# Kernel tuning notes

Hardware: AMD Instinct MI355X
Metric: run time of the kernel (lower is better)

## Reference

```python
import jax, jax.numpy as jnp
import numpy as np

N_NODES = 50000   # gnn_nodes_num
N_EDGES = 800000  # avg degree 16
HIDDEN = 64       # hidden_channels
BATCH_Y = 2048    # |y|


def setup_inputs() -> dict:
    key = jax.random.key(0)
    ks = jax.random.split(key, 16)
    s = 0.05
    H = HIDDEN
    return {
        "x": jnp.arange(N_NODES, dtype=jnp.int32),
        "edge_index": jax.random.randint(ks[0], (2, N_EDGES), 0, N_NODES, dtype=jnp.int32),
        "y": jax.random.randint(ks[1], (BATCH_Y,), 0, N_NODES, dtype=jnp.int32),
        # learned params
        "emb": jax.random.normal(ks[2], (N_NODES, H), dtype=jnp.float32) * s,
        "Wq": jax.random.normal(ks[3], (H, H), dtype=jnp.float32) * s,
        "bq": jnp.zeros((H,), dtype=jnp.float32),
        "Wk": jax.random.normal(ks[4], (H, H), dtype=jnp.float32) * s,
        "bk": jnp.zeros((H,), dtype=jnp.float32),
        "Wv": jax.random.normal(ks[5], (H, H), dtype=jnp.float32) * s,
        "bv": jnp.zeros((H,), dtype=jnp.float32),
        "Ws": jax.random.normal(ks[6], (H, H), dtype=jnp.float32) * s,  # root/skip lin
        "bs": jnp.zeros((H,), dtype=jnp.float32),
        "W1": jax.random.normal(ks[7], (H, N_NODES), dtype=jnp.float32) * s,
        "b1": jnp.zeros((N_NODES,), dtype=jnp.float32),
    }


def reference(x, edge_index, y, emb, Wq, bq, Wk, bk, Wv, bv, Ws, bs, W1, b1):
    H = Wq.shape[1]
    h = emb[x]                                  # [N, H] embedding lookup
    src, dst = edge_index[0], edge_index[1]

    # TransformerConv (heads=1, root_weight=True): per-node projections
    q = h @ Wq + bq                             # [N, H]
    k = h @ Wk + bk
    v = h @ Wv + bv

    # attention logits per edge, softmax grouped by destination node
    logits = jnp.sum(q[dst] * k[src], axis=-1) / jnp.sqrt(jnp.float32(H))  # [E]
    m = jax.ops.segment_max(logits, dst, num_segments=N_NODES)             # [N]
    e = jnp.exp(logits - m[dst])
    denom = jax.ops.segment_sum(e, dst, num_segments=N_NODES)              # [N]
    alpha = e / denom[dst]                                                 # [E]

    agg = jax.ops.segment_sum(alpha[:, None] * v[src], dst, num_segments=N_NODES)
    out = agg + h @ Ws + bs                     # [N, H] GAT output

    # for each node u: sum of out[dst] over edges with src == u  (vectorized
    # form of the original per-y boolean-mask loop), then gather at y
    neigh = jax.ops.segment_sum(out[dst], src, num_segments=N_NODES)       # [N, H]
    new_x = neigh[y]                            # [B, H]

    return jax.nn.softmax(new_x @ W1 + b1, axis=-1)  # [B, N]
```

## Files before the change

### kernel.cpp

```cpp
#include <hip/hip_runtime.h>
#include <math.h>

#define NN 50000
#define NE 800000
#define HH 64
#define NB 2048
#define NTILES 784
#define NPAD 50176
#define NSTRIPE 64
#define NBLK 256

typedef __attribute__((ext_vector_type(8))) short bf16x8;
typedef __attribute__((ext_vector_type(4))) float f32x4;

__device__ inline ushort f2bf(float f) {
  uint u = __float_as_uint(f);
  uint r = (u + 0x7fffu + ((u >> 16) & 1u)) >> 16;
  return (ushort)r;
}
__device__ inline float bf2f(uint u) { return __uint_as_float(u << 16); }

__global__ __launch_bounds__(256) void k_prep(
    const float* __restrict__ W1,
    const float* __restrict__ Wq, const float* __restrict__ Wk,
    const float* __restrict__ Wv, const float* __restrict__ Ws,
    ushort* __restrict__ W1T, ushort* __restrict__ WT,
    int* cnt_d, int* cnt_s, char* flag, char* ymark, int* bar)
{
  int i = blockIdx.x * 256 + threadIdx.x;
  if (i < NN) { cnt_d[i] = 0; cnt_s[i] = 0; flag[i] = 0; ymark[i] = 0; }
  if (i == 0) *bar = 0;
  if (i < 4 * HH * HH) {
    int m = i >> 12, rem = i & 4095;
    int c = rem >> 6, kk = rem & 63;
    const float* W = (m == 0) ? Wq : (m == 1) ? Wk : (m == 2) ? Wv : Ws;
    WT[i] = f2bf(W[kk * HH + c]);
  }
  if (i < NPAD) {
    uint4 o[8];
    ushort* op = (ushort*)o;
    if (i < NN) {
#pragma unroll
      for (int k = 0; k < HH; ++k) op[k] = f2bf(W1[(size_t)k * NN + i]);
    } else {
#pragma unroll
      for (int k = 0; k < HH; ++k) op[k] = 0;
    }
    uint4* dst = (uint4*)(W1T + (size_t)i * HH);
#pragma unroll
    for (int j = 0; j < 8; ++j) dst[j] = o[j];
  }
}

__global__ __launch_bounds__(256) void k_mark(const int* __restrict__ y,
                                              char* __restrict__ ymark) {
  int i = blockIdx.x * 256 + threadIdx.x;
  if (i < NB) ymark[y[i]] = 1;
}

__global__ __launch_bounds__(256) void k_hist(const int* __restrict__ src,
                                              const int* __restrict__ dst,
                                              const char* __restrict__ ymark,
                                              int* cnt_s, int* cnt_d,
                                              char* __restrict__ flag,
                                              int* __restrict__ rank_d,
                                              int* __restrict__ rank_s) {
  int e = blockIdx.x * 256 + threadIdx.x;
  if (e < NE) {
    int s = src[e], d = dst[e];
    rank_d[e] = atomicAdd(&cnt_d[d], 1);
    if (ymark[s]) {
      rank_s[e] = atomicAdd(&cnt_s[s], 1);
      flag[d] = 1;
    } else {
      rank_s[e] = -1;
    }
  }
}

__global__ __launch_bounds__(1024) void k_scan(
    const int* __restrict__ cnt_d, int* indptr_d,
    const int* __restrict__ cnt_s, int* indptr_s)
{
  const int* cnt = (blockIdx.x == 0) ? cnt_d : cnt_s;
  int* indptr    = (blockIdx.x == 0) ? indptr_d : indptr_s;
  __shared__ int sums[1024];
  const int CH = (NN + 1023) / 1024;
  int t = threadIdx.x;
  int begin = t * CH;
  int end = begin + CH; if (end > NN) end = NN;
  int s = 0;
  for (int i = begin; i < end; ++i) s += cnt[i];
  sums[t] = s;
  __syncthreads();
  for (int off = 1; off < 1024; off <<= 1) {
    int val = (t >= off) ? sums[t - off] : 0;
    __syncthreads();
    sums[t] += val;
    __syncthreads();
  }
  int prefix = (t == 0) ? 0 : sums[t - 1];
  for (int i = begin; i < end; ++i) {
    indptr[i] = prefix;
    prefix += cnt[i];
  }
  if (t == 0) indptr[NN] = sums[1023];
}

__global__ __launch_bounds__(256) void k_qkvs(
    const int* __restrict__ x, const float* __restrict__ emb,
    const ushort* __restrict__ WT,
    const float* __restrict__ bq, const float* __restrict__ bk,
    const float* __restrict__ bv, const float* __restrict__ bs,
    ushort* __restrict__ qb, ushort* __restrict__ kb, ushort* __restrict__ vb,
    float* __restrict__ hs)
{
  int l = threadIdx.x & 63, w = threadIdx.x >> 6;
  int lr = l & 15, lk = l >> 4;
  int r0 = blockIdx.x * 64;
  const ushort* wt = WT + w * HH * HH;
  const float* B = (w == 0) ? bq : (w == 1) ? bk : (w == 2) ? bv : bs;

  bf16x8 b[2][4];
#pragma unroll
  for (int kt = 0; kt < 2; ++kt)
#pragma unroll
    for (int nt = 0; nt < 4; ++nt)
      b[kt][nt] = *(const bf16x8*)(wt + (nt * 16 + lr) * HH + kt * 32 + lk * 8);

  bf16x8 a[2][4];
#pragma unroll
  for (int mt = 0; mt < 4; ++mt) {
    int row = r0 + mt * 16 + lr;
    int g = (row < NN) ? x[row] : 0;
    const float* hp = emb + (size_t)g * HH;
#pragma unroll
    for (int kt = 0; kt < 2; ++kt) {
      float4 f0 = *(const float4*)(hp + kt * 32 + lk * 8);
      float4 f1 = *(const float4*)(hp + kt * 32 + lk * 8 + 4);
      bf16x8 af;
      af[0] = f2bf(f0.x); af[1] = f2bf(f0.y); af[2] = f2bf(f0.z); af[3] = f2bf(f0.w);
      af[4] = f2bf(f1.x); af[5] = f2bf(f1.y); af[6] = f2bf(f1.z); af[7] = f2bf(f1.w);
      a[kt][mt] = af;
    }
  }

  f32x4 acc[4][4];
  const f32x4 z4 = {0.f, 0.f, 0.f, 0.f};
#pragma unroll
  for (int mt = 0; mt < 4; ++mt)
#pragma unroll
    for (int nt = 0; nt < 4; ++nt) acc[mt][nt] = z4;
#pragma unroll
  for (int kt = 0; kt < 2; ++kt)
#pragma unroll
    for (int mt = 0; mt < 4; ++mt)
#pragma unroll
      for (int nt = 0; nt < 4; ++nt)
        acc[mt][nt] = __builtin_amdgcn_mfma_f32_16x16x32_bf16(a[kt][mt], b[kt][nt], acc[mt][nt], 0, 0, 0);

  if (w < 3) {
    ushort* Db = (w == 0) ? qb : (w == 1) ? kb : vb;
#pragma unroll
    for (int mt = 0; mt < 4; ++mt)
#pragma unroll
      for (int r = 0; r < 4; ++r) {
        int row = r0 + mt * 16 + lk * 4 + r;
        if (row < NN) {
#pragma unroll
          for (int nt = 0; nt < 4; ++nt) {
            int c = nt * 16 + lr;
            Db[(size_t)row * HH + c] = f2bf(acc[mt][nt][r] + B[c]);
          }
        }
      }
  } else {
#pragma unroll
    for (int mt = 0; mt < 4; ++mt)
#pragma unroll
      for (int r = 0; r < 4; ++r) {
        int row = r0 + mt * 16 + lk * 4 + r;
        if (row < NN) {
#pragma unroll
          for (int nt = 0; nt < 4; ++nt) {
            int c = nt * 16 + lr;
            hs[(size_t)row * HH + c] = acc[mt][nt][r] + B[c];
          }
        }
      }
  }
}

__global__ __launch_bounds__(256) void k_efill(
    const int* __restrict__ src, const int* __restrict__ dst,
    const ushort* __restrict__ qb, const ushort* __restrict__ kb,
    const char* __restrict__ flag,
    const int* __restrict__ indptr_s, const int* __restrict__ indptr_d,
    const int* __restrict__ rank_d, const int* __restrict__ rank_s,
    int* __restrict__ dstlist_s, int2* __restrict__ slot_d)
{
  int gid = blockIdx.x * 256 + threadIdx.x;
  int e = gid >> 3;
  int lane = gid & 7;
  if (e >= NE) return;
  int s = src[e], d = dst[e];
  bool fd = flag[d];
  float p = 0.f;
  if (fd) {
    uint4 qa = *(const uint4*)(qb + (size_t)d * HH + lane * 8);
    uint4 ka = *(const uint4*)(kb + (size_t)s * HH + lane * 8);
    p += bf2f(qa.x & 0xffffu) * bf2f(ka.x & 0xffffu) + bf2f(qa.x >> 16) * bf2f(ka.x >> 16);
    p += bf2f(qa.y & 0xffffu) * bf2f(ka.y & 0xffffu) + bf2f(qa.y >> 16) * bf2f(ka.y >> 16);
    p += bf2f(qa.z & 0xffffu) * bf2f(ka.z & 0xffffu) + bf2f(qa.z >> 16) * bf2f(ka.z >> 16);
    p += bf2f(qa.w & 0xffffu) * bf2f(ka.w & 0xffffu) + bf2f(qa.w >> 16) * bf2f(ka.w >> 16);
    p += __shfl_xor(p, 4);
    p += __shfl_xor(p, 2);
    p += __shfl_xor(p, 1);
  }
  if (lane == 0) {
    if (fd) {
      int pd = indptr_d[d] + rank_d[e];
      int2 sl; sl.x = s; sl.y = __float_as_int(p * 0.125f);
      slot_d[pd] = sl;
    }
    int rs = rank_s[e];
    if (rs >= 0) dstlist_s[indptr_s[s] + rs] = d;
  }
}

__global__ __launch_bounds__(256) void k_agg(
    const int* __restrict__ indptr_d, const int2* __restrict__ slot_d,
    const ushort* __restrict__ vb, const char* __restrict__ flag,
    float* __restrict__ hs)
{
  int w = (blockIdx.x * 256 + threadIdx.x) >> 6;
  int lane = threadIdx.x & 63;
  if (w >= NN) return;
  if (!flag[w]) return;
  int beg = indptr_d[w], end = indptr_d[w + 1];
  if (beg == end) return;
  float den = 0.f, acc = 0.f;
  for (int j = beg; j < end; ++j) {
    int2 sl = slot_d[j];
    float p = __expf(__int_as_float(sl.y));
    den += p;
    acc = fmaf(p, bf2f((uint)vb[(size_t)sl.x * HH + lane]), acc);
  }
  hs[(size_t)w * HH + lane] += acc / den;
}

__global__ __launch_bounds__(256) void k_newx(
    const int* __restrict__ y, const int* __restrict__ indptr_s,
    const int* __restrict__ dstlist_s, const float* __restrict__ outn,
    ushort* __restrict__ nxbf)
{
  int w = (blockIdx.x * 256 + threadIdx.x) >> 6;
  int lane = threadIdx.x & 63;
  if (w >= NB) return;
  int u = y[w];
  int beg = indptr_s[u], end = indptr_s[u + 1];
  float acc = 0.f;
  for (int j = beg; j < end; ++j) acc += outn[(size_t)dstlist_s[j] * HH + lane];
  nxbf[w * HH + lane] = f2bf(acc);
}

#define LOADA(A, t) do { int bn0_ = (t) * 64;                                    \
  _Pragma("unroll") for (int kt = 0; kt < 2; ++kt)                               \
  _Pragma("unroll") for (int nt = 0; nt < 4; ++nt)                               \
    A[kt][nt] = *(const bf16x8*)(w1t + (size_t)(bn0_ + nt * 16 + lr) * HH + kt * 32 + lk * 8); \
} while (0)

#define MFMA16(A, acc) do {                                                      \
  _Pragma("unroll") for (int kt = 0; kt < 2; ++kt)                               \
  _Pragma("unroll") for (int mt = 0; mt < 4; ++mt)                               \
  _Pragma("unroll") for (int nt = 0; nt < 4; ++nt)                               \
    acc[mt][nt] = __builtin_amdgcn_mfma_f32_16x16x32_bf16(A[kt][nt], bm[kt][mt], acc[mt][nt], 0, 0, 0); \
} while (0)

#define PROCA(A, t) do { int bn0_ = (t) * 64;                                    \
  f32x4 acc[4][4];                                                               \
  _Pragma("unroll") for (int mt = 0; mt < 4; ++mt)                               \
  _Pragma("unroll") for (int nt = 0; nt < 4; ++nt) acc[mt][nt] = z4;             \
  MFMA16(A, acc);                                                                \
  _Pragma("unroll") for (int nt = 0; nt < 4; ++nt) {                             \
    int n0 = bn0_ + nt * 16 + lk * 4;                                            \
    if (n0 < NN) {                                                               \
      f32x4 bb = *(const f32x4*)(b1 + n0);                                       \
      _Pragma("unroll") for (int mt = 0; mt < 4; ++mt)                           \
      _Pragma("unroll") for (int r = 0; r < 4; ++r)                              \
        se[mt] += __expf(acc[mt][nt][r] + bb[r]);                                \
    } }                                                                          \
} while (0)

#define PROCB(A, t) do { int bn0_ = (t) * 64;                                    \
  f32x4 acc[4][4];                                                               \
  _Pragma("unroll") for (int mt = 0; mt < 4; ++mt)                               \
  _Pragma("unroll") for (int nt = 0; nt < 4; ++nt) acc[mt][nt] = z4;             \
  MFMA16(A, acc);                                                                \
  _Pragma("unroll") for (int nt = 0; nt < 4; ++nt) {                             \
    int n0 = bn0_ + nt * 16 + lk * 4;                                            \
    if (n0 < NN) {                                                               \
      f32x4 bb = *(const f32x4*)(b1 + n0);                                       \
      _Pragma("unroll") for (int mt = 0; mt < 4; ++mt) {                         \
        int row = bm0 + mt * 16 + lr;                                            \
        f32x4 vx;                                                                \
        _Pragma("unroll") for (int r = 0; r < 4; ++r)                            \
          vx[r] = __expf(acc[mt][nt][r] + bb[r]) * sv[mt];                       \
        __builtin_nontemporal_store(vx, (f32x4*)(out + (size_t)row * NN + n0));  \
      }                                                                          \
    } }                                                                          \
} while (0)

__global__ __launch_bounds__(512, 1) void k_final(
    const ushort* __restrict__ nxbf, const ushort* __restrict__ w1t,
    const float* __restrict__ b1, float* __restrict__ Spart,
    int* __restrict__ bar, float* __restrict__ out)
{
  __shared__ float sInvS[512];
  int tid = threadIdx.x;
  int l = tid & 63, w = tid >> 6;
  int lr = l & 15, lk = l >> 4;
  int rg = blockIdx.x >> 6;
  int st = blockIdx.x & 63;
  int bm0 = rg * 512 + w * 64;
  const f32x4 z4 = {0.f, 0.f, 0.f, 0.f};

  bf16x8 bm[2][4];
#pragma unroll
  for (int kt = 0; kt < 2; ++kt)
#pragma unroll
    for (int mt = 0; mt < 4; ++mt)
      bm[kt][mt] = *(const bf16x8*)(nxbf + (size_t)(bm0 + mt * 16 + lr) * HH + kt * 32 + lk * 8);

  float se[4];
#pragma unroll
  for (int mt = 0; mt < 4; ++mt) se[mt] = 0.f;

  {
    bf16x8 aA[2][4], aB[2][4];
    int t = st;
    LOADA(aA, t);
    while (true) {
      int t1 = t + NSTRIPE;
      if (t1 < NTILES) LOADA(aB, t1);
      PROCA(aA, t);
      if (t1 >= NTILES) break;
      int t2 = t1 + NSTRIPE;
      if (t2 < NTILES) LOADA(aA, t2);
      PROCA(aB, t1);
      if (t2 >= NTILES) break;
      t = t2;
    }
  }

#pragma unroll
  for (int mt = 0; mt < 4; ++mt) {
    float s = se[mt];
    s += __shfl_xor(s, 16);
    s += __shfl_xor(s, 32);
    if (lk == 0) {
      int row = bm0 + mt * 16 + lr;
      __hip_atomic_store(&Spart[row * NSTRIPE + st], s,
                         __ATOMIC_RELAXED, __HIP_MEMORY_SCOPE_AGENT);
    }
  }

  __threadfence();
  __syncthreads();
  if (tid == 0) {
    __hip_atomic_fetch_add(bar, 1, __ATOMIC_ACQ_REL, __HIP_MEMORY_SCOPE_AGENT);
    while (__hip_atomic_load(bar, __ATOMIC_ACQUIRE, __HIP_MEMORY_SCOPE_AGENT) < NBLK)
      __builtin_amdgcn_s_sleep(2);
  }
  __syncthreads();

  {
    int row = rg * 512 + tid;
    float s = 0.f;
    for (int j = 0; j < NSTRIPE; ++j)
      s += __hip_atomic_load(&Spart[row * NSTRIPE + j],
                             __ATOMIC_RELAXED, __HIP_MEMORY_SCOPE_AGENT);
    sInvS[tid] = 1.0f / s;
  }
  __syncthreads();

  float sv[4];
#pragma unroll
  for (int mt = 0; mt < 4; ++mt) sv[mt] = sInvS[w * 64 + mt * 16 + lr];

  {
    bf16x8 aA[2][4], aB[2][4];
    int t = st;
    LOADA(aA, t);
    while (true) {
      int t1 = t + NSTRIPE;
      if (t1 < NTILES) LOADA(aB, t1);
      PROCB(aA, t);
      if (t1 >= NTILES) break;
      int t2 = t1 + NSTRIPE;
      if (t2 < NTILES) LOADA(aA, t2);
      PROCB(aB, t1);
      if (t2 >= NTILES) break;
      t = t2;
    }
  }
}

extern "C" void kernel_launch(void* const* d_in, const int* in_sizes, int n_in,
                              void* d_out, int out_size, void* d_ws, size_t ws_size,
                              hipStream_t stream)
{
  const int* x   = (const int*)d_in[0];
  const int* src = (const int*)d_in[1];
  const int* dst = src + NE;
  const int* y   = (const int*)d_in[2];
  const float* emb = (const float*)d_in[3];
  const float* Wq = (const float*)d_in[4];  const float* bq = (const float*)d_in[5];
  const float* Wk = (const float*)d_in[6];  const float* bk = (const float*)d_in[7];
  const float* Wv = (const float*)d_in[8];  const float* bv = (const float*)d_in[9];
  const float* Ws = (const float*)d_in[10]; const float* bs = (const float*)d_in[11];
  const float* W1 = (const float*)d_in[12]; const float* b1 = (const float*)d_in[13];
  float* out = (float*)d_out;

  char* wsb = (char*)d_ws;
  ushort* nxbf  = (ushort*)wsb;
  ushort* w1t   = (ushort*)(wsb + 262144);
  float*  Spart = (float*)(wsb + 6684672);
  int*    bar   = (int*)(wsb + 7208960);
  const size_t PERS  = 7209088;
  const size_t BIGSZ = 46400000;
  char* big = (ws_size >= PERS + BIGSZ) ? (wsb + PERS) : (char*)d_out;
  ushort* qb     = (ushort*)(big + 0);
  ushort* kb     = (ushort*)(big + 6400000);
  ushort* vb     = (ushort*)(big + 12800000);
  float*  hs     = (float*)(big + 19200000);
  int2*   slot_d = (int2*)(big + 32000000);
  int* dstlist_s = (int*)(big + 38400000);
  int* rank_d    = (int*)(big + 38700000);
  int* rank_s    = (int*)(big + 41900000);
  int* cnt_d     = (int*)(big + 45100000);
  int* cnt_s     = (int*)(big + 45300000);
  int* indptr_d  = (int*)(big + 45500000);
  int* indptr_s  = (int*)(big + 45700064);
  char* flag     = (char*)(big + 45900128);
  char* ymark    = (char*)(big + 45950176);
  ushort* WT     = (ushort*)(big + 46000224);

  k_prep<<<dim3(224), dim3(256), 0, stream>>>(W1, Wq, Wk, Wv, Ws, w1t, WT,
                                              cnt_d, cnt_s, flag, ymark, bar);
  k_mark<<<dim3(8), dim3(256), 0, stream>>>(y, ymark);
  k_hist<<<dim3(3125), dim3(256), 0, stream>>>(src, dst, ymark, cnt_s, cnt_d,
                                               flag, rank_d, rank_s);
  k_scan<<<dim3(2), dim3(1024), 0, stream>>>(cnt_d, indptr_d, cnt_s, indptr_s);
  k_qkvs<<<dim3(782), dim3(256), 0, stream>>>(x, emb, WT, bq, bk, bv, bs,
                                              qb, kb, vb, hs);
  k_efill<<<dim3(25000), dim3(256), 0, stream>>>(src, dst, qb, kb, flag,
                                                 indptr_s, indptr_d, rank_d, rank_s,
                                                 dstlist_s, slot_d);
  k_agg<<<dim3(12500), dim3(256), 0, stream>>>(indptr_d, slot_d, vb, flag, hs);
  k_newx<<<dim3(512), dim3(256), 0, stream>>>(y, indptr_s, dstlist_s, hs, nxbf);
  k_final<<<dim3(NBLK), dim3(512), 0, stream>>>(nxbf, w1t, b1, Spart, bar, out);
}
```

Baseline: 512.9 us.

## Split fused softmax-GEMM into three kernels and stage output through LDS

Replaces the single persistent k_final kernel, which used a grid-wide spin barrier, with three launches. k_finA computes partial exp-sums, k_sinv reduces them to inverse row sums, and k_finB recomputes the GEMM and writes the normalized output. Each warp now owns 16 rows instead of 64, and the column range is split into 16 contiguous stripes of 49 tiles. k_finB transposes results through swizzled LDS so each lane stores contiguous row segments, in place of scattered nontemporal column stores. This removes the barrier and improves store coalescing, at the cost of two extra launches, more reloads of W1T per row, and plain rather than nontemporal stores.

Result: no change. 505.8 us (-1.4%).

```diff
diff --git a/kernel.cpp b/kernel.cpp
--- a/kernel.cpp
+++ b/kernel.cpp
@@ -5,10 +5,10 @@
 #define NE 800000
 #define HH 64
 #define NB 2048
-#define NTILES 784
 #define NPAD 50176
-#define NSTRIPE 64
-#define NBLK 256
+#define NST 16
+#define TPS 49
+#define NSUP 12
 
 typedef __attribute__((ext_vector_type(8))) short bf16x8;
 typedef __attribute__((ext_vector_type(4))) float f32x4;
@@ -25,11 +25,10 @@
     const float* __restrict__ Wq, const float* __restrict__ Wk,
     const float* __restrict__ Wv, const float* __restrict__ Ws,
     ushort* __restrict__ W1T, ushort* __restrict__ WT,
-    int* cnt_d, int* cnt_s, char* flag, char* ymark, int* bar)
+    int* cnt_d, int* cnt_s, char* flag, char* ymark)
 {
   int i = blockIdx.x * 256 + threadIdx.x;
   if (i < NN) { cnt_d[i] = 0; cnt_s[i] = 0; flag[i] = 0; ymark[i] = 0; }
-  if (i == 0) *bar = 0;
   if (i < 4 * HH * HH) {
     int m = i >> 12, rem = i & 4095;
     int c = rem >> 6, kk = rem & 63;
@@ -270,138 +269,148 @@
     A[kt][nt] = *(const bf16x8*)(w1t + (size_t)(bn0_ + nt * 16 + lr) * HH + kt * 32 + lk * 8); \
 } while (0)
 
-#define MFMA16(A, acc) do {                                                      \
+#define MFMA8(A, acc) do {                                                       \
   _Pragma("unroll") for (int kt = 0; kt < 2; ++kt)                               \
-  _Pragma("unroll") for (int mt = 0; mt < 4; ++mt)                               \
   _Pragma("unroll") for (int nt = 0; nt < 4; ++nt)                               \
-    acc[mt][nt] = __builtin_amdgcn_mfma_f32_16x16x32_bf16(A[kt][nt], bm[kt][mt], acc[mt][nt], 0, 0, 0); \
+    acc[nt] = __builtin_amdgcn_mfma_f32_16x16x32_bf16(A[kt][nt], bm[kt], acc[nt], 0, 0, 0); \
 } while (0)
 
 #define PROCA(A, t) do { int bn0_ = (t) * 64;                                    \
-  f32x4 acc[4][4];                                                               \
-  _Pragma("unroll") for (int mt = 0; mt < 4; ++mt)                               \
-  _Pragma("unroll") for (int nt = 0; nt < 4; ++nt) acc[mt][nt] = z4;             \
-  MFMA16(A, acc);                                                                \
+  f32x4 acc[4];                                                                  \
+  _Pragma("unroll") for (int nt = 0; nt < 4; ++nt) acc[nt] = z4;                 \
+  MFMA8(A, acc);                                                                 \
   _Pragma("unroll") for (int nt = 0; nt < 4; ++nt) {                             \
     int n0 = bn0_ + nt * 16 + lk * 4;                                            \
     if (n0 < NN) {                                                               \
       f32x4 bb = *(const f32x4*)(b1 + n0);                                       \
-      _Pragma("unroll") for (int mt = 0; mt < 4; ++mt)                           \
       _Pragma("unroll") for (int r = 0; r < 4; ++r)                              \
-        se[mt] += __expf(acc[mt][nt][r] + bb[r]);                                \
+        se += __expf(acc[nt][r] + bb[r]);                                        \
     } }                                                                          \
 } while (0)
 
-#define PROCB(A, t) do { int bn0_ = (t) * 64;                                    \
-  f32x4 acc[4][4];                                                               \
-  _Pragma("unroll") for (int mt = 0; mt < 4; ++mt)                               \
-  _Pragma("unroll") for (int nt = 0; nt < 4; ++nt) acc[mt][nt] = z4;             \
-  MFMA16(A, acc);                                                                \
-  _Pragma("unroll") for (int nt = 0; nt < 4; ++nt) {                             \
-    int n0 = bn0_ + nt * 16 + lk * 4;                                            \
-    if (n0 < NN) {                                                               \
-      f32x4 bb = *(const f32x4*)(b1 + n0);                                       \
-      _Pragma("unroll") for (int mt = 0; mt < 4; ++mt) {                         \
-        int row = bm0 + mt * 16 + lr;                                            \
-        f32x4 vx;                                                                \
-        _Pragma("unroll") for (int r = 0; r < 4; ++r)                            \
-          vx[r] = __expf(acc[mt][nt][r] + bb[r]) * sv[mt];                       \
-        __builtin_nontemporal_store(vx, (f32x4*)(out + (size_t)row * NN + n0));  \
-      }                                                                          \
-    } }                                                                          \
-} while (0)
-
-__global__ __launch_bounds__(512, 1) void k_final(
+__global__ __launch_bounds__(256) void k_finA(
     const ushort* __restrict__ nxbf, const ushort* __restrict__ w1t,
-    const float* __restrict__ b1, float* __restrict__ Spart,
-    int* __restrict__ bar, float* __restrict__ out)
-{
-  __shared__ float sInvS[512];
+    const float* __restrict__ b1, float* __restrict__ Spart)
+{
   int tid = threadIdx.x;
   int l = tid & 63, w = tid >> 6;
   int lr = l & 15, lk = l >> 4;
-  int rg = blockIdx.x >> 6;
-  int st = blockIdx.x & 63;
-  int bm0 = rg * 512 + w * 64;
+  int b = blockIdx.x;
+  int st = ((b & 7) << 1) | ((b >> 3) & 1);
+  int r0 = (b >> 4) * 64 + w * 16;
+  int tile0 = st * TPS;
   const f32x4 z4 = {0.f, 0.f, 0.f, 0.f};
 
-  bf16x8 bm[2][4];
+  bf16x8 bm[2];
 #pragma unroll
   for (int kt = 0; kt < 2; ++kt)
-#pragma unroll
-    for (int mt = 0; mt < 4; ++mt)
-      bm[kt][mt] = *(const bf16x8*)(nxbf + (size_t)(bm0 + mt * 16 + lr) * HH + kt * 32 + lk * 8);
-
-  float se[4];
-#pragma unroll
-  for (int mt = 0; mt < 4; ++mt) se[mt] = 0.f;
-
+    bm[kt] = *(const bf16x8*)(nxbf + (size_t)(r0 + lr) * HH + kt * 32 + lk * 8);
+
+  float se = 0.f;
   {
-    bf16x8 aA[2][4], aB[2][4];
-    int t = st;
-    LOADA(aA, t);
-    while (true) {
-      int t1 = t + NSTRIPE;
-      if (t1 < NTILES) LOADA(aB, t1);
-      PROCA(aA, t);
-      if (t1 >= NTILES) break;
-      int t2 = t1 + NSTRIPE;
-      if (t2 < NTILES) LOADA(aA, t2);
-      PROCA(aB, t1);
-      if (t2 >= NTILES) break;
-      t = t2;
-    }
-  }
-
-#pragma unroll
-  for (int mt = 0; mt < 4; ++mt) {
-    float s = se[mt];
-    s += __shfl_xor(s, 16);
-    s += __shfl_xor(s, 32);
-    if (lk == 0) {
-      int row = bm0 + mt * 16 + lr;
-      __hip_atomic_store(&Spart[row * NSTRIPE + st], s,
-                         __ATOMIC_RELAXED, __HIP_MEMORY_SCOPE_AGENT);
-    }
-  }
-
-  __threadfence();
-  __syncthreads();
-  if (tid == 0) {
-    __hip_atomic_fetch_add(bar, 1, __ATOMIC_ACQ_REL, __HIP_MEMORY_SCOPE_AGENT);
-    while (__hip_atomic_load(bar, __ATOMIC_ACQUIRE, __HIP_MEMORY_SCOPE_AGENT) < NBLK)
-      __builtin_amdgcn_s_sleep(2);
-  }
-  __syncthreads();
-
+    bf16x8 A0[2][4], A1[2][4];
+    LOADA(A0, tile0);
+#pragma unroll 4
+    for (int t = 0; t < TPS - 1; t += 2) {
+      LOADA(A1, tile0 + t + 1);
+      PROCA(A0, tile0 + t);
+      LOADA(A0, tile0 + t + 2);
+      PROCA(A1, tile0 + t + 1);
+    }
+    PROCA(A0, tile0 + TPS - 1);
+  }
+  se += __shfl_xor(se, 16);
+  se += __shfl_xor(se, 32);
+  if (lk == 0) Spart[(r0 + lr) * NST + st] = se;
+}
+
+__global__ __launch_bounds__(256) void k_sinv(const float* __restrict__ Spart,
+                                              float* __restrict__ Sinv) {
+  int r = blockIdx.x * 256 + threadIdx.x;
+  if (r < NB) {
+    float s = 0.f;
+#pragma unroll
+    for (int j = 0; j < NST; ++j) s += Spart[r * NST + j];
+    Sinv[r] = 1.0f / s;
+  }
+}
+
+#define PROCB1(A, t, tt) do { int bn0_ = (t) * 64;                               \
+  f32x4 acc[4];                                                                  \
+  _Pragma("unroll") for (int nt = 0; nt < 4; ++nt) acc[nt] = z4;                 \
+  MFMA8(A, acc);                                                                 \
+  _Pragma("unroll") for (int nt = 0; nt < 4; ++nt) {                             \
+    int n0 = bn0_ + nt * 16 + lk * 4;                                            \
+    f32x4 bb = (n0 < NN) ? *(const f32x4*)(b1 + n0) : z4;                        \
+    f32x4 ev;                                                                    \
+    _Pragma("unroll") for (int r = 0; r < 4; ++r)                                \
+      ev[r] = __expf(acc[nt][r] + bb[r]) * sv;                                   \
+    int col = (tt) * 64 + nt * 16 + lk * 4;                                      \
+    *(f32x4*)&lw[lr * 256 + (col ^ ((lr & 7) << 2))] = ev;                       \
+  }                                                                              \
+} while (0)
+
+__global__ __launch_bounds__(256) void k_finB(
+    const ushort* __restrict__ nxbf, const ushort* __restrict__ w1t,
+    const float* __restrict__ b1, const float* __restrict__ Sinv,
+    float* __restrict__ out)
+{
+  __shared__ float lt[4 * 4096];
+  int tid = threadIdx.x;
+  int l = tid & 63, w = tid >> 6;
+  int lr = l & 15, lk = l >> 4;
+  int b = blockIdx.x;
+  int st = ((b & 7) << 1) | ((b >> 3) & 1);
+  int r0 = (b >> 4) * 64 + w * 16;
+  int tile0 = st * TPS;
+  const f32x4 z4 = {0.f, 0.f, 0.f, 0.f};
+  float* lw = &lt[w * 4096];
+
+  bf16x8 bm[2];
+#pragma unroll
+  for (int kt = 0; kt < 2; ++kt)
+    bm[kt] = *(const bf16x8*)(nxbf + (size_t)(r0 + lr) * HH + kt * 32 + lk * 8);
+
+  float sv = Sinv[r0 + lr];
+
+  for (int sb = 0; sb < NSUP; ++sb) {
+    int tb = tile0 + sb * 4;
+    bf16x8 A0[2][4], A1[2][4];
+    LOADA(A0, tb);
+    LOADA(A1, tb + 1);
+    PROCB1(A0, tb, 0);
+    LOADA(A0, tb + 2);
+    PROCB1(A1, tb + 1, 1);
+    LOADA(A1, tb + 3);
+    PROCB1(A0, tb + 2, 2);
+    PROCB1(A1, tb + 3, 3);
+    int nbase = tb * 64 + l * 4;
+#pragma unroll
+    for (int i = 0; i < 16; ++i) {
+      f32x4 vx = *(const f32x4*)&lw[i * 256 + ((l * 4) ^ ((i & 7) << 2))];
+      if (nbase < NN)
+        *(f32x4*)(out + (size_t)(r0 + i) * NN + nbase) = vx;
+    }
+  }
   {
-    int row = rg * 512 + tid;
-    float s = 0.f;
-    for (int j = 0; j < NSTRIPE; ++j)
-      s += __hip_atomic_load(&Spart[row * NSTRIPE + j],
-                             __ATOMIC_RELAXED, __HIP_MEMORY_SCOPE_AGENT);
-    sInvS[tid] = 1.0f / s;
-  }
-  __syncthreads();
-
-  float sv[4];
-#pragma unroll
-  for (int mt = 0; mt < 4; ++mt) sv[mt] = sInvS[w * 64 + mt * 16 + lr];
-
-  {
-    bf16x8 aA[2][4], aB[2][4];
-    int t = st;
-    LOADA(aA, t);
-    while (true) {
-      int t1 = t + NSTRIPE;
-      if (t1 < NTILES) LOADA(aB, t1);
-      PROCB(aA, t);
-      if (t1 >= NTILES) break;
-      int t2 = t1 + NSTRIPE;
-      if (t2 < NTILES) LOADA(aA, t2);
-      PROCB(aB, t1);
-      if (t2 >= NTILES) break;
-      t = t2;
+    int t = tile0 + TPS - 1;
+    int bn0 = t * 64;
+    bf16x8 A0[2][4];
+    LOADA(A0, t);
+    f32x4 acc[4];
+#pragma unroll
+    for (int nt = 0; nt < 4; ++nt) acc[nt] = z4;
+    MFMA8(A0, acc);
+#pragma unroll
+    for (int nt = 0; nt < 4; ++nt) {
+      int n0 = bn0 + nt * 16 + lk * 4;
+      if (n0 < NN) {
+        f32x4 bb = *(const f32x4*)(b1 + n0);
+        f32x4 vx;
+#pragma unroll
+        for (int r = 0; r < 4; ++r) vx[r] = __expf(acc[nt][r] + bb[r]) * sv;
+        *(f32x4*)(out + (size_t)(r0 + lr) * NN + n0) = vx;
+      }
     }
   }
 }
@@ -426,8 +435,8 @@
   ushort* nxbf  = (ushort*)wsb;
   ushort* w1t   = (ushort*)(wsb + 262144);
   float*  Spart = (float*)(wsb + 6684672);
-  int*    bar   = (int*)(wsb + 7208960);
-  const size_t PERS  = 7209088;
+  float*  Sinv  = (float*)(wsb + 6815744);
+  const size_t PERS  = 6823936;
   const size_t BIGSZ = 46400000;
   char* big = (ws_size >= PERS + BIGSZ) ? (wsb + PERS) : (char*)d_out;
   ushort* qb     = (ushort*)(big + 0);
@@ -447,7 +456,7 @@
   ushort* WT     = (ushort*)(big + 46000224);
 
   k_prep<<<dim3(224), dim3(256), 0, stream>>>(W1, Wq, Wk, Wv, Ws, w1t, WT,
-                                              cnt_d, cnt_s, flag, ymark, bar);
+                                              cnt_d, cnt_s, flag, ymark);
   k_mark<<<dim3(8), dim3(256), 0, stream>>>(y, ymark);
   k_hist<<<dim3(3125), dim3(256), 0, stream>>>(src, dst, ymark, cnt_s, cnt_d,
                                                flag, rank_d, rank_s);
@@ -459,5 +468,7 @@
                                                  dstlist_s, slot_d);
   k_agg<<<dim3(12500), dim3(256), 0, stream>>>(indptr_d, slot_d, vb, flag, hs);
   k_newx<<<dim3(512), dim3(256), 0, stream>>>(y, indptr_s, dstlist_s, hs, nxbf);
-  k_final<<<dim3(NBLK), dim3(512), 0, stream>>>(nxbf, w1t, b1, Spart, bar, out);
-}
+  k_finA<<<dim3(512), dim3(256), 0, stream>>>(nxbf, w1t, b1, Spart);
+  k_sinv<<<dim3(8), dim3(256), 0, stream>>>(Spart, Sinv);
+  k_finB<<<dim3(512), dim3(256), 0, stream>>>(nxbf, w1t, b1, Sinv, out);
+}
```
